# Optimization experiments

Hardware: AMD Instinct MI355X
Metric: run time of the kernel (lower is better)

Reference implementation:

```python
import jax, jax.numpy as jnp
import numpy as np

B, C, H, W = 16, 512, 32, 32
COND_C, L_COND = 768, 77
N_GROUPS, N_HEADS = 8, 8
HEAD = C // N_HEADS
EPS = 1e-5


def setup_inputs() -> dict:
    key = jax.random.key(0)
    ks = jax.random.split(key, 6)
    s = lambda fan_in: 1.0 / np.sqrt(fan_in)
    return {
        "x_0": jax.random.normal(ks[0], (B, C, H, W), jnp.float32),
        "cond": jax.random.normal(ks[1], (B, L_COND, COND_C), jnp.float32),
        "gn_gamma": jnp.ones((C,), jnp.float32),
        "gn_beta": jnp.zeros((C,), jnp.float32),
        "qkv_w": jax.random.normal(ks[2], (3 * C, C), jnp.float32) * s(C),
        "qkv_b": jnp.zeros((3 * C,), jnp.float32),
        "cond_kv_w": jax.random.normal(ks[3], (2 * C, COND_C), jnp.float32) * s(COND_C),
        "cond_kv_b": jnp.zeros((2 * C,), jnp.float32),
        "out_w": jax.random.normal(ks[4], (C, C), jnp.float32) * s(C),
        "out_b": jnp.zeros((C,), jnp.float32),
    }


def reference(x_0, cond, gn_gamma, gn_beta, qkv_w, qkv_b, cond_kv_w, cond_kv_b, out_w, out_b):
    b, c, h, w = x_0.shape
    L = h * w
    # --- GroupNorm over (C/G, H, W) per group, per-channel affine ---
    xg = x_0.reshape(b, N_GROUPS, c // N_GROUPS, h * w)
    mu = xg.mean(axis=(2, 3), keepdims=True)
    var = xg.var(axis=(2, 3), keepdims=True)
    xn = ((xg - mu) * jax.lax.rsqrt(var + EPS)).reshape(b, c, h, w)
    xn = xn * gn_gamma[None, :, None, None] + gn_beta[None, :, None, None]
    # --- to tokens [B, L, C] ---
    x = xn.transpose(0, 2, 3, 1).reshape(b, L, c)
    # --- QKV ---
    qkv = x @ qkv_w.T + qkv_b  # [B, L, 3C]
    q, k, v = jnp.split(qkv, 3, axis=-1)
    q = q.reshape(b, L, N_HEADS, HEAD)
    k = k.reshape(b, L, N_HEADS, HEAD)
    v = v.reshape(b, L, N_HEADS, HEAD)
    # --- conditional K/V ---
    kv_c = cond @ cond_kv_w.T + cond_kv_b  # [B, Lc, 2C]
    k_c, v_c = jnp.split(kv_c, 2, axis=-1)
    Lc = cond.shape[1]
    k_c = k_c.reshape(b, Lc, N_HEADS, HEAD)
    v_c = v_c.reshape(b, Lc, N_HEADS, HEAD)
    K = jnp.concatenate([k, k_c], axis=1)  # [B, L+Lc, H, D]
    V = jnp.concatenate([v, v_c], axis=1)
    # --- attention (full score matrix, as in the original) ---
    scale = HEAD ** -0.5
    scores = jnp.einsum("bqhd,bkhd->bhqk", q, K) * scale
    att = jax.nn.softmax(scores, axis=-1)
    out = jnp.einsum("bhqk,bkhd->bqhd", att, V).reshape(b, L, c)
    out = out @ out_w.T + out_b
    # --- back to image + residual ---
    out = out.reshape(b, h, w, c).transpose(0, 3, 1, 2)
    return out + x_0
```

## Files before the change

kernel.cpp:

```cpp
#include <hip/hip_runtime.h>

typedef short bf16x8 __attribute__((ext_vector_type(8)));
typedef float f32x4 __attribute__((ext_vector_type(4)));
typedef float f32x16 __attribute__((ext_vector_type(16)));
typedef unsigned int u32x4 __attribute__((ext_vector_type(4)));

#define KVP 1152

__device__ __forceinline__ unsigned short f2b(float f) {
    unsigned int u = __float_as_uint(f);
    u += 0x7FFFu + ((u >> 16) & 1u);
    return (unsigned short)(u >> 16);
}

__device__ __forceinline__ f32x4 mfma16(bf16x8 a, bf16x8 b, f32x4 c) {
    return __builtin_amdgcn_mfma_f32_16x16x32_bf16(a, b, c, 0, 0, 0);
}
__device__ __forceinline__ f32x16 mfma32(bf16x8 a, bf16x8 b, f32x16 c) {
    return __builtin_amdgcn_mfma_f32_32x32x16_bf16(a, b, c, 0, 0, 0);
}
__device__ __forceinline__ float exp2_raw(float x) {
    float r; asm("v_exp_f32 %0, %1" : "=v"(r) : "v"(x)); return r;
}
__device__ __forceinline__ unsigned cvt_pk(float lo, float hi) {
    unsigned r; asm("v_cvt_pk_bf16_f32 %0, %1, %2" : "=v"(r) : "v"(lo), "v"(hi)); return r;
}

typedef __attribute__((address_space(3))) unsigned int lds_u32_t;
typedef const __attribute__((address_space(1))) unsigned int glb_u32_t;
__device__ __forceinline__ void async_cp16(const void* g, void* l) {
    __builtin_amdgcn_global_load_lds((glb_u32_t*)(unsigned long long)g,
                                     (lds_u32_t*)(unsigned int)(unsigned long long)l,
                                     16, 0, 0);
}

__global__ __launch_bounds__(256) void gn_stats_k(const float* __restrict__ x, float* __restrict__ stats) {
    int bg = blockIdx.x;
    const float4* p = (const float4*)(x + (size_t)bg * 64 * 1024);
    float s = 0.f, ss = 0.f;
    for (int i = threadIdx.x; i < 16384; i += 256) {
        float4 v = p[i];
        s  += v.x + v.y + v.z + v.w;
        ss += v.x * v.x + v.y * v.y + v.z * v.z + v.w * v.w;
    }
#pragma unroll
    for (int o = 32; o; o >>= 1) { s += __shfl_down(s, o); ss += __shfl_down(ss, o); }
    __shared__ float red[8];
    int w = threadIdx.x >> 6;
    if ((threadIdx.x & 63) == 0) { red[w] = s; red[4 + w] = ss; }
    __syncthreads();
    if (threadIdx.x == 0) {
        s  = red[0] + red[1] + red[2] + red[3];
        ss = red[4] + red[5] + red[6] + red[7];
        float mean = s * (1.f / 65536.f);
        float var  = ss * (1.f / 65536.f) - mean * mean;
        stats[2 * bg]     = mean;
        stats[2 * bg + 1] = rsqrtf(var + 1e-5f);
    }
}

__global__ __launch_bounds__(256) void gn_apply_k(const float* __restrict__ x, const float* __restrict__ stats,
                                                  const float* __restrict__ gamma, const float* __restrict__ beta,
                                                  unsigned short* __restrict__ xt) {
    int st = blockIdx.x & 15;
    int ct = (blockIdx.x >> 4) & 7;
    int b  = blockIdx.x >> 7;
    float mean = stats[2 * (b * 8 + ct)];
    float rsig = stats[2 * (b * 8 + ct) + 1];
    __shared__ unsigned short tile[64][65];
    int tid = threadIdx.x;
#pragma unroll
    for (int it = 0; it < 4; ++it) {
        int idx = it * 256 + tid;
        int ci = idx >> 4, j4 = idx & 15;
        int c = ct * 64 + ci;
        float4 v = *(const float4*)(x + ((size_t)b * 512 + c) * 1024 + st * 64 + j4 * 4);
        float gs = gamma[c] * rsig;
        float bo = beta[c] - mean * gs;
        tile[j4 * 4 + 0][ci] = f2b(v.x * gs + bo);
        tile[j4 * 4 + 1][ci] = f2b(v.y * gs + bo);
        tile[j4 * 4 + 2][ci] = f2b(v.z * gs + bo);
        tile[j4 * 4 + 3][ci] = f2b(v.w * gs + bo);
    }
    __syncthreads();
#pragma unroll
    for (int it = 0; it < 4; ++it) {
        int idx = it * 256 + tid;
        int si = idx >> 4, q = idx & 15;
        uint2 u;
        u.x = (unsigned)tile[si][q * 4 + 0] | ((unsigned)tile[si][q * 4 + 1] << 16);
        u.y = (unsigned)tile[si][q * 4 + 2] | ((unsigned)tile[si][q * 4 + 3] << 16);
        *(uint2*)(xt + ((size_t)b * 1024 + st * 64 + si) * 512 + ct * 64 + q * 4) = u;
    }
}

__global__ __launch_bounds__(256) void cvt_k(const float* __restrict__ in, unsigned short* __restrict__ out, int n4) {
    int i = blockIdx.x * 256 + threadIdx.x;
    if (i < n4) {
        float4 v = ((const float4*)in)[i];
        uint2 u;
        u.x = (unsigned)f2b(v.x) | ((unsigned)f2b(v.y) << 16);
        u.y = (unsigned)f2b(v.z) | ((unsigned)f2b(v.w) << 16);
        ((uint2*)out)[i] = u;
    }
}

template <int EPI>
__global__ __launch_bounds__(256) void gemm128_k(const unsigned short* __restrict__ A,
                                                 const unsigned short* __restrict__ Bw,
                                                 const float* __restrict__ bias,
                                                 int M, int N, int K,
                                                 unsigned short* __restrict__ Qo,
                                                 unsigned short* __restrict__ Ko,
                                                 unsigned short* __restrict__ Vo,
                                                 const float* __restrict__ x0,
                                                 float* __restrict__ outp) {
    __shared__ __align__(16) unsigned short As[2][4096];
    __shared__ __align__(16) unsigned short Bs[2][4096];
    const int m0 = blockIdx.x * 128, n0 = blockIdx.y * 128;
    const int tid = threadIdx.x, lane = tid & 63, w = tid >> 6;
    const int wr = w >> 1, wc = w & 1;
    const int lc = lane & 15, lg = lane >> 4;

    const int sRow = lane >> 2;
    const int sSlot = (lane & 3) ^ ((lane >> 3) & 3);
    const unsigned short* aSrc0 = A + (size_t)(m0 + 16 * w + sRow) * K + sSlot * 8;
    const unsigned short* aSrc1 = A + (size_t)(m0 + 64 + 16 * w + sRow) * K + sSlot * 8;
    const unsigned short* bSrc0 = Bw + (size_t)(n0 + 16 * w + sRow) * K + sSlot * 8;
    const unsigned short* bSrc1 = Bw + (size_t)(n0 + 64 + 16 * w + sRow) * K + sSlot * 8;

    const int rSlot8 = (lg ^ ((lc >> 1) & 3)) * 8;

    f32x4 acc[4][4];
#pragma unroll
    for (int m = 0; m < 4; ++m)
#pragma unroll
        for (int n = 0; n < 4; ++n) acc[m][n] = (f32x4){0.f, 0.f, 0.f, 0.f};

    const int nT = K >> 5;
    {
        async_cp16(aSrc0, &As[0][w * 512]);
        async_cp16(aSrc1, &As[0][(4 + w) * 512]);
        async_cp16(bSrc0, &Bs[0][w * 512]);
        async_cp16(bSrc1, &Bs[0][(4 + w) * 512]);
    }
    __syncthreads();

    for (int t = 0; t < nT; ++t) {
        const int cur = t & 1;
        if (t + 1 < nT) {
            const int k1 = (t + 1) << 5;
            async_cp16(aSrc0 + k1, &As[cur ^ 1][w * 512]);
            async_cp16(aSrc1 + k1, &As[cur ^ 1][(4 + w) * 512]);
            async_cp16(bSrc0 + k1, &Bs[cur ^ 1][w * 512]);
            async_cp16(bSrc1 + k1, &Bs[cur ^ 1][(4 + w) * 512]);
        }
        bf16x8 af[4], bfr[4];
#pragma unroll
        for (int m = 0; m < 4; ++m)
            af[m] = *(const bf16x8*)&As[cur][(wr * 64 + m * 16 + lc) * 32 + rSlot8];
#pragma unroll
        for (int n = 0; n < 4; ++n)
            bfr[n] = *(const bf16x8*)&Bs[cur][(wc * 64 + n * 16 + lc) * 32 + rSlot8];
#pragma unroll
        for (int m = 0; m < 4; ++m)
#pragma unroll
            for (int n = 0; n < 4; ++n)
                acc[m][n] = mfma16(af[m], bfr[n], acc[m][n]);
        __syncthreads();
    }

#pragma unroll
    for (int n = 0; n < 4; ++n) {
        int col = n0 + wc * 64 + n * 16 + lc;
        float bv = bias[col];
#pragma unroll
        for (int m = 0; m < 4; ++m) {
            int rb = m0 + wr * 64 + m * 16 + lg * 4;
#pragma unroll
            for (int r = 0; r < 4; ++r) {
                int token = rb + r;
                float val = acc[m][n][r] + bv;
                if (EPI == 0) {
                    int b = token >> 10, l = token & 1023;
                    if (col < 512) {
                        int hh = col >> 6, d = col & 63;
                        Qo[((size_t)(b * 8 + hh) * 1024 + l) * 64 + d] = f2b(val * (0.125f * 1.44269504089f));
                    } else if (col < 1024) {
                        int j = col - 512, hh = j >> 6, d = j & 63;
                        Ko[((size_t)(b * 8 + hh) * KVP + l) * 64 + d] = f2b(val);
                    } else {
                        int j = col - 1024, hh = j >> 6, d = j & 63;
                        Vo[((size_t)(b * 8 + hh) * 64 + d) * KVP + l] = f2b(val);
                    }
                } else {
                    int b = token >> 10, hw = token & 1023;
                    size_t a = ((size_t)b * 512 + col) * 1024 + hw;
                    outp[a] = val + x0[a];
                }
            }
        }
    }
}

__global__ __launch_bounds__(256) void gemm_nt_k(const unsigned short* __restrict__ A,
                                                 const unsigned short* __restrict__ Bw,
                                                 const float* __restrict__ bias,
                                                 int M, int N, int K,
                                                 unsigned short* __restrict__ Ko,
                                                 unsigned short* __restrict__ Vo) {
    __shared__ unsigned short As[64][40];
    __shared__ unsigned short Bs[64][40];
    const int m0 = blockIdx.x * 64, n0 = blockIdx.y * 64;
    const int tid = threadIdx.x, lane = tid & 63, w = tid >> 6;
    const int lc = lane & 15, lg = lane >> 4;
    const int lrow = tid >> 2, lseg = tid & 3;
    f32x4 acc[4];
#pragma unroll
    for (int i = 0; i < 4; ++i) acc[i] = (f32x4){0.f, 0.f, 0.f, 0.f};

    for (int k0 = 0; k0 < K; k0 += 32) {
        uint4 av = make_uint4(0u, 0u, 0u, 0u);
        if (m0 + lrow < M) av = *(const uint4*)(A + (size_t)(m0 + lrow) * K + k0 + lseg * 8);
        *(uint4*)&As[lrow][lseg * 8] = av;
        uint4 bv = *(const uint4*)(Bw + (size_t)(n0 + lrow) * K + k0 + lseg * 8);
        *(uint4*)&Bs[lrow][lseg * 8] = bv;
        __syncthreads();
        bf16x8 af = *(const bf16x8*)&As[w * 16 + lc][lg * 8];
#pragma unroll
        for (int ct = 0; ct < 4; ++ct) {
            bf16x8 bfr = *(const bf16x8*)&Bs[ct * 16 + lc][lg * 8];
            acc[ct] = mfma16(af, bfr, acc[ct]);
        }
        __syncthreads();
    }

    const int rbase = m0 + w * 16 + lg * 4;
#pragma unroll
    for (int ct = 0; ct < 4; ++ct) {
        int col = n0 + ct * 16 + lc;
        float bv = bias[col];
#pragma unroll
        for (int r = 0; r < 4; ++r) {
            int token = rbase + r;
            if (token >= M) continue;
            float val = acc[ct][r] + bv;
            int b = token / 77, l = token - b * 77;
            if (col < 512) {
                int hh = col >> 6, d = col & 63;
                Ko[((size_t)(b * 8 + hh) * KVP + 1024 + l) * 64 + d] = f2b(val);
            } else {
                int j = col - 512, hh = j >> 6, d = j & 63;
                Vo[((size_t)(b * 8 + hh) * 64 + d) * KVP + 1024 + l] = f2b(val);
            }
        }
    }
}

__global__ __launch_bounds__(512) void attn2_k(const unsigned short* __restrict__ Q,
                                               const unsigned short* __restrict__ Kb,
                                               const unsigned short* __restrict__ Vt,
                                               unsigned short* __restrict__ atok) {
    __shared__ __align__(16) unsigned short lds[18432];

    const int bh = blockIdx.x >> 2;
    const int qt = blockIdx.x & 3;
    const int w  = threadIdx.x >> 6;
    const int lane = threadIdx.x & 63;
    const int ql = lane & 31, hi = lane >> 5;
    const int q0 = qt * 256 + w * 32;

    bf16x8 qf[4];
    const unsigned short* Qp = Q + ((size_t)bh * 1024 + q0 + ql) * 64 + hi * 8;
#pragma unroll
    for (int ks = 0; ks < 4; ++ks) qf[ks] = *(const bf16x8*)(Qp + ks * 16);

    const unsigned short* Kg = Kb + (size_t)bh * KVP * 64;
    const unsigned short* Vg = Vt + (size_t)bh * 64 * KVP;

    const int srow = lane >> 3;
    const int sc   = (((lane & 7) ^ (lane >> 3)) << 3);

    f32x16 o0, o1;
#pragma unroll
    for (int i = 0; i < 16; ++i) { o0[i] = 0.f; o1[i] = 0.f; }
    float mreg = -1e30f, lsum = 0.f;

    {
        uint4 kr = *(const uint4*)(Kg + (size_t)(8 * w + srow) * 64 + sc);
        uint4 vr = *(const uint4*)(Vg + (size_t)(8 * w + srow) * KVP + sc);
        *(uint4*)&lds[w * 512 + lane * 8] = kr;
        *(uint4*)&lds[4096 + w * 512 + lane * 8] = vr;
    }
    __syncthreads();

    int cur = 0;
    for (int it = 0; it < 18; ++it) {
        const int kv0 = it * 64;
        const bool pre = (it < 17);
        uint4 kn, vn;
        if (pre) {
            kn = *(const uint4*)(Kg + (size_t)(kv0 + 64 + 8 * w + srow) * 64 + sc);
            vn = *(const uint4*)(Vg + (size_t)(8 * w + srow) * KVP + kv0 + 64 + sc);
        }
        const int kb = cur * 8192, vb = cur * 8192 + 4096;

        f32x16 s0, s1;
#pragma unroll
        for (int i = 0; i < 16; ++i) { s0[i] = 0.f; s1[i] = 0.f; }
#pragma unroll
        for (int ks = 0; ks < 4; ++ks) {
            const int sl = ((ks * 2 + hi) ^ (ql & 7)) << 3;
            bf16x8 kf0 = *(const bf16x8*)&lds[kb + ql * 64 + sl];
            bf16x8 kf1 = *(const bf16x8*)&lds[kb + (32 + ql) * 64 + sl];
            s0 = mfma32(kf0, qf[ks], s0);
            s1 = mfma32(kf1, qf[ks], s1);
        }
        if (kv0 == 1088) {
#pragma unroll
            for (int r = 0; r < 16; ++r) {
                int kva = 1088 + (r & 3) + 8 * (r >> 2) + 4 * hi;
                if (kva >= 1101) s0[r] = -1e30f;
                if (kva + 32 >= 1101) s1[r] = -1e30f;
            }
        }

        float t[16];
#pragma unroll
        for (int i = 0; i < 16; ++i) t[i] = fmaxf(s0[i], s1[i]);
#pragma unroll
        for (int st = 8; st; st >>= 1)
#pragma unroll
            for (int i = 0; i < st; ++i) t[i] = fmaxf(t[i], t[i + st]);
        float pmax = fmaxf(t[0], __shfl_xor(t[0], 32));

        if (__any(pmax > mreg + 8.f)) {
            float mn = fmaxf(mreg, pmax);
            float al = exp2_raw(mreg - mn);
            mreg = mn;
            lsum *= al;
#pragma unroll
            for (int i = 0; i < 16; ++i) { o0[i] *= al; o1[i] *= al; }
        }

        unsigned pk0[8], pk1[8];
        float sA = 0.f, sB = 0.f, sC = 0.f, sD = 0.f;
#pragma unroll
        for (int i = 0; i < 8; ++i) {
            float a0 = exp2_raw(s0[2 * i] - mreg), a1 = exp2_raw(s0[2 * i + 1] - mreg);
            float b0 = exp2_raw(s1[2 * i] - mreg), b1 = exp2_raw(s1[2 * i + 1] - mreg);
            pk0[i] = cvt_pk(a0, a1);
            pk1[i] = cvt_pk(b0, b1);
            sA += a0; sB += a1; sC += b0; sD += b1;
        }
        float ls = (sA + sB) + (sC + sD);
        ls += __shfl_xor(ls, 32);
        lsum += ls;

#pragma unroll
        for (int t2 = 0; t2 < 2; ++t2) {
            const unsigned* pk = t2 ? pk1 : pk0;
#pragma unroll
            for (int v = 0; v < 2; ++v) {
                unsigned a0 = pk[4 * v], a1 = pk[4 * v + 1], a2 = pk[4 * v + 2], a3 = pk[4 * v + 3];
                unsigned x = __shfl_xor(hi ? a0 : a2, 32);
                unsigned y = __shfl_xor(hi ? a1 : a3, 32);
                u32x4 fw;
                fw.x = hi ? x : a0; fw.y = hi ? y : a1; fw.z = hi ? a2 : x; fw.w = hi ? a3 : y;
                bf16x8 pf = __builtin_bit_cast(bf16x8, fw);
                const int ks2 = 2 * t2 + v;
                const int sl = ((ks2 * 2 + hi) ^ (ql & 7)) << 3;
                bf16x8 vf0 = *(const bf16x8*)&lds[vb + ql * 64 + sl];
                bf16x8 vf1 = *(const bf16x8*)&lds[vb + (32 + ql) * 64 + sl];
                o0 = mfma32(vf0, pf, o0);
                o1 = mfma32(vf1, pf, o1);
            }
        }

        if (pre) {
            *(uint4*)&lds[(cur ^ 1) * 8192 + w * 512 + lane * 8] = kn;
            *(uint4*)&lds[(cur ^ 1) * 8192 + 4096 + w * 512 + lane * 8] = vn;
        }
        __syncthreads();
        cur ^= 1;
    }

    float rinv = 1.f / lsum;
    unsigned short* sw = &lds[w * 2304];
#pragma unroll
    for (int dt = 0; dt < 2; ++dt) {
#pragma unroll
        for (int rp = 0; rp < 8; ++rp) {
            float e0 = (dt ? o1[2 * rp] : o0[2 * rp]) * rinv;
            float e1 = (dt ? o1[2 * rp + 1] : o0[2 * rp + 1]) * rinv;
            int d = dt * 32 + ((2 * rp) & 3) + 8 * ((2 * rp) >> 2) + 4 * hi;
            *(unsigned*)&sw[ql * 72 + d] = cvt_pk(e0, e1);
        }
    }
    __syncthreads();
    {
        int i = threadIdx.x >> 1, hf = threadIdx.x & 1;
        const unsigned short* src = &lds[(i >> 5) * 2304 + (i & 31) * 72 + hf * 32];
        u32x4 r0 = *(const u32x4*)(src);
        u32x4 r1 = *(const u32x4*)(src + 8);
        u32x4 r2 = *(const u32x4*)(src + 16);
        u32x4 r3 = *(const u32x4*)(src + 24);
        int b = bh >> 3, h = bh & 7;
        unsigned short* gd = atok + ((size_t)b * 1024 + qt * 256 + i) * 512 + h * 64 + hf * 32;
        *(u32x4*)(gd) = r0;
        *(u32x4*)(gd + 8) = r1;
        *(u32x4*)(gd + 16) = r2;
        *(u32x4*)(gd + 24) = r3;
    }
}

extern "C" void kernel_launch(void* const* d_in, const int* in_sizes, int n_in,
                              void* d_out, int out_size, void* d_ws, size_t ws_size,
                              hipStream_t stream) {
    const float* x0     = (const float*)d_in[0];
    const float* cond   = (const float*)d_in[1];
    const float* gamma  = (const float*)d_in[2];
    const float* beta   = (const float*)d_in[3];
    const float* qkv_w  = (const float*)d_in[4];
    const float* qkv_b  = (const float*)d_in[5];
    const float* ckv_w  = (const float*)d_in[6];
    const float* ckv_b  = (const float*)d_in[7];
    const float* out_w  = (const float*)d_in[8];
    const float* out_b  = (const float*)d_in[9];
    float* outp = (float*)d_out;

    char* p = (char*)d_ws;
    float* stats = (float*)p;            p += 1024;
    unsigned short* xt    = (unsigned short*)p; p += (size_t)16384 * 512 * 2;
    unsigned short* wqkv  = (unsigned short*)p; p += (size_t)1536 * 512 * 2;
    unsigned short* wckv  = (unsigned short*)p; p += (size_t)1024 * 768 * 2;
    unsigned short* wout  = (unsigned short*)p; p += (size_t)512 * 512 * 2;
    unsigned short* condb = (unsigned short*)p; p += (size_t)1232 * 768 * 2;
    unsigned short* Qb    = (unsigned short*)p; p += (size_t)16 * 8 * 1024 * 64 * 2;
    unsigned short* Kb    = (unsigned short*)p; p += (size_t)16 * 8 * KVP * 64 * 2;
    unsigned short* Vtb   = (unsigned short*)p; p += (size_t)16 * 8 * KVP * 64 * 2;
    unsigned short* atok  = (unsigned short*)p; p += (size_t)16384 * 512 * 2;

    gn_stats_k<<<128, 256, 0, stream>>>(x0, stats);
    gn_apply_k<<<2048, 256, 0, stream>>>(x0, stats, gamma, beta, xt);
    cvt_k<<<768, 256, 0, stream>>>(qkv_w, wqkv, 196608);
    cvt_k<<<768, 256, 0, stream>>>(ckv_w, wckv, 196608);
    cvt_k<<<256, 256, 0, stream>>>(out_w, wout, 65536);
    cvt_k<<<924, 256, 0, stream>>>(cond, condb, 236544);

    gemm128_k<0><<<dim3(128, 12), 256, 0, stream>>>(xt, wqkv, qkv_b, 16384, 1536, 512,
                                                    Qb, Kb, Vtb, nullptr, nullptr);
    gemm_nt_k<<<dim3(20, 16), 256, 0, stream>>>(condb, wckv, ckv_b, 1232, 1024, 768, Kb, Vtb);
    attn2_k<<<512, 512, 0, stream>>>(Qb, Kb, Vtb, atok);
    gemm128_k<2><<<dim3(128, 4), 256, 0, stream>>>(atok, wout, out_b, 16384, 512, 512,
                                                   nullptr, nullptr, nullptr, x0, outp);
}
```

Baseline: 195.5 us.

## Triple-buffer GEMM shared-memory tiles with explicit vmcnt waits

Turns the double-buffered async global-to-LDS pipeline in the 128x128 GEMM into a three-stage ring that prefetches two k-tiles ahead. The single __syncthreads is replaced by explicit s_waitcnt vmcnt counts, raw s_barriers and a sched_barrier, so loads for later tiles can stay in flight while the current tile is computed. The intent is to hide global-memory latency. In exchange it uses more LDS per block, which may lower occupancy, adds a second barrier per iteration, and depends on the hand-written vmcnt counts matching the number of async copies issued.

```diff
diff --git a/kernel.cpp b/kernel.cpp
--- a/kernel.cpp
+++ b/kernel.cpp
@@ -115,8 +115,8 @@
                                                  unsigned short* __restrict__ Vo,
                                                  const float* __restrict__ x0,
                                                  float* __restrict__ outp) {
-    __shared__ __align__(16) unsigned short As[2][4096];
-    __shared__ __align__(16) unsigned short Bs[2][4096];
+    __shared__ __align__(16) unsigned short As[3][4096];
+    __shared__ __align__(16) unsigned short Bs[3][4096];
     const int m0 = blockIdx.x * 128, n0 = blockIdx.y * 128;
     const int tid = threadIdx.x, lane = tid & 63, w = tid >> 6;
     const int wr = w >> 1, wc = w & 1;
@@ -138,36 +138,51 @@
         for (int n = 0; n < 4; ++n) acc[m][n] = (f32x4){0.f, 0.f, 0.f, 0.f};
 
     const int nT = K >> 5;
-    {
-        async_cp16(aSrc0, &As[0][w * 512]);
-        async_cp16(aSrc1, &As[0][(4 + w) * 512]);
-        async_cp16(bSrc0, &Bs[0][w * 512]);
-        async_cp16(bSrc1, &Bs[0][(4 + w) * 512]);
-    }
-    __syncthreads();
-
+    async_cp16(aSrc0, &As[0][w * 512]);
+    async_cp16(aSrc1, &As[0][(4 + w) * 512]);
+    async_cp16(bSrc0, &Bs[0][w * 512]);
+    async_cp16(bSrc1, &Bs[0][(4 + w) * 512]);
+    async_cp16(aSrc0 + 32, &As[1][w * 512]);
+    async_cp16(aSrc1 + 32, &As[1][(4 + w) * 512]);
+    async_cp16(bSrc0 + 32, &Bs[1][w * 512]);
+    async_cp16(bSrc1 + 32, &Bs[1][(4 + w) * 512]);
+
+    int c = 0;
+#pragma unroll 1
     for (int t = 0; t < nT; ++t) {
-        const int cur = t & 1;
-        if (t + 1 < nT) {
-            const int k1 = (t + 1) << 5;
-            async_cp16(aSrc0 + k1, &As[cur ^ 1][w * 512]);
-            async_cp16(aSrc1 + k1, &As[cur ^ 1][(4 + w) * 512]);
-            async_cp16(bSrc0 + k1, &Bs[cur ^ 1][w * 512]);
-            async_cp16(bSrc1 + k1, &Bs[cur ^ 1][(4 + w) * 512]);
-        }
+        if (t + 2 < nT) {
+            int c2 = c + 2; if (c2 >= 3) c2 -= 3;
+            const int k2 = (t + 2) << 5;
+            async_cp16(aSrc0 + k2, &As[c2][w * 512]);
+            async_cp16(aSrc1 + k2, &As[c2][(4 + w) * 512]);
+            async_cp16(bSrc0 + k2, &Bs[c2][w * 512]);
+            async_cp16(bSrc1 + k2, &Bs[c2][(4 + w) * 512]);
+            asm volatile("s_waitcnt vmcnt(8)" ::: "memory");
+        } else if (t + 1 < nT) {
+            asm volatile("s_waitcnt vmcnt(4)" ::: "memory");
+        } else {
+            asm volatile("s_waitcnt vmcnt(0)" ::: "memory");
+        }
+        __builtin_amdgcn_s_barrier();
+
         bf16x8 af[4], bfr[4];
 #pragma unroll
         for (int m = 0; m < 4; ++m)
-            af[m] = *(const bf16x8*)&As[cur][(wr * 64 + m * 16 + lc) * 32 + rSlot8];
+            af[m] = *(const bf16x8*)&As[c][(wr * 64 + m * 16 + lc) * 32 + rSlot8];
 #pragma unroll
         for (int n = 0; n < 4; ++n)
-            bfr[n] = *(const bf16x8*)&Bs[cur][(wc * 64 + n * 16 + lc) * 32 + rSlot8];
+            bfr[n] = *(const bf16x8*)&Bs[c][(wc * 64 + n * 16 + lc) * 32 + rSlot8];
+        asm volatile("s_waitcnt lgkmcnt(0)" ::: "memory");
+        __builtin_amdgcn_sched_barrier(0);
+        __builtin_amdgcn_s_barrier();
+
 #pragma unroll
         for (int m = 0; m < 4; ++m)
 #pragma unroll
             for (int n = 0; n < 4; ++n)
                 acc[m][n] = mfma16(af[m], bfr[n], acc[m][n]);
-        __syncthreads();
+
+        ++c; if (c == 3) c = 0;
     }
 
 #pragma unroll
```

Result: faster. 187.8 us (-3.9%).
